# Kernel tuning notes

Hardware: AMD Instinct MI355X
Metric: run time of the kernel (lower is better)

Reference implementation:

```python
import jax, jax.numpy as jnp
import numpy as np

DIM = 784
HEADS = 2
DH = DIM // HEADS  # 392
EPS_LN = 1e-5
EPS_L2 = 1e-12


def layer_norm(x, w, b):
    mu = jnp.mean(x, axis=-1, keepdims=True)
    var = jnp.mean(jnp.square(x - mu), axis=-1, keepdims=True)
    return (x - mu) * jax.lax.rsqrt(var + EPS_LN) * w + b


def hardswish(x):
    return x * jnp.clip(x + 3.0, 0.0, 6.0) / 6.0


def l2norm(x):
    n = jnp.sqrt(jnp.sum(jnp.square(x), axis=-1, keepdims=True))
    return x / jnp.maximum(n, EPS_L2)


def setup_inputs() -> dict:
    key = jax.random.key(0)
    ks = jax.random.split(key, 8)
    B, N = 32, 1024
    x = jax.random.normal(ks[0], (B, N, DIM), dtype=jnp.float32)
    s = 0.02
    qkv_w = jax.random.normal(ks[1], (3 * DIM, DIM), dtype=jnp.float32) * s
    qkv_b = jax.random.normal(ks[2], (3 * DIM,), dtype=jnp.float32) * s
    out_w = jax.random.normal(ks[3], (DIM, DIM), dtype=jnp.float32) * s
    out_b = jax.random.normal(ks[4], (DIM,), dtype=jnp.float32) * s
    ffn_w = jax.random.normal(ks[5], (DIM, DIM), dtype=jnp.float32) * s
    ffn_b = jax.random.normal(ks[6], (DIM,), dtype=jnp.float32) * s
    ln_w = jnp.ones((DIM,), dtype=jnp.float32)
    ln_b = jnp.zeros((DIM,), dtype=jnp.float32)
    scale = jnp.ones((HEADS, 1, 1), dtype=jnp.float32) * 0.01
    return {"x": x, "ln_w": ln_w, "ln_b": ln_b, "qkv_w": qkv_w, "qkv_b": qkv_b,
            "scale": scale, "out_w": out_w, "out_b": out_b, "ffn_w": ffn_w, "ffn_b": ffn_b}


def reference(x, ln_w, ln_b, qkv_w, qkv_b, scale, out_w, out_b, ffn_w, ffn_b):
    B, N, _ = x.shape
    h = HEADS
    xn = layer_norm(x, ln_w, ln_b)
    qkv = xn @ qkv_w.T + qkv_b  # [B, N, 3*DIM]
    q, k, v = jnp.split(qkv, 3, axis=-1)
    # 'b n (h d) -> b h n d'
    def to_heads(t):
        return t.reshape(B, N, h, DH).transpose(0, 2, 1, 3)
    q, k, v = to_heads(q), to_heads(k), to_heads(v)
    q, k = l2norm(q), l2norm(k)
    sim = jnp.einsum('bhnd,bhmd->bhnm', q, k) * jnp.sqrt(scale)  # scale [h,1,1] broadcasts
    attn = jax.nn.softmax(sim, axis=-1)
    out = jnp.einsum('bhnm,bhmd->bhnd', attn, v)
    out = out.transpose(0, 2, 1, 3).reshape(B, N, DIM)  # 'b h n d -> b n (h d)'
    out = layer_norm(out, ln_w, ln_b)  # same LayerNorm params reused
    out = hardswish(out)
    out_ffn = hardswish(out @ ffn_w.T + ffn_b)
    return (out + out_ffn) @ out_w.T + out_b
```

## Files before the change

kernel.cpp:

```cpp
#include <hip/hip_runtime.h>

typedef unsigned short u16;
typedef unsigned int u32;
typedef __attribute__((ext_vector_type(4))) float f32x4;
typedef __attribute__((ext_vector_type(8))) short bf16x8;

#define TOK 32768
#define KP  832
#define DHP 448
#define DHPV 512
#define NQKV 2560

static __device__ __forceinline__ float bf2f(u16 u){ u32 v = ((u32)u)<<16; return __builtin_bit_cast(float, v); }
static __device__ __forceinline__ u16 f2bf(float f){
  u32 x = __builtin_bit_cast(u32, f);
  u32 r = (x + 0x7fffu + ((x>>16)&1u)) >> 16;
  return (u16)r;
}
static __device__ __forceinline__ void gload16(const void* g, void* l){
  __builtin_amdgcn_global_load_lds((const __attribute__((address_space(1))) void*)g,
                                   (__attribute__((address_space(3))) void*)l, 16, 0, 0);
}
static __device__ __forceinline__ float wave_red_sum(float v){
  #pragma unroll
  for (int o = 32; o > 0; o >>= 1) v += __shfl_xor(v, o, 64);
  return v;
}

__global__ __launch_bounds__(256) void wconv_k(const float* __restrict__ src, u16* __restrict__ dst,
                                               int srcR, long long total){
  long long i = (long long)blockIdx.x*256 + threadIdx.x;
  if (i >= total) return;
  int r = (int)(i / KP), c = (int)(i % KP);
  float v = (r < srcR && c < 784) ? src[(long long)r*784 + c] : 0.f;
  dst[i] = f2bf(v);
}

__global__ __launch_bounds__(256) void ln1_k(const float* __restrict__ x, const float* __restrict__ w,
                                             const float* __restrict__ b, u16* __restrict__ out){
  const int tid = threadIdx.x;
  const long long row = blockIdx.x;
  const float* xr = x + row*784;
  float v[4]; float s = 0.f, ss = 0.f;
  #pragma unroll
  for (int i = 0; i < 4; i++){ int c = tid + i*256; float t = (c < 784) ? xr[c] : 0.f; v[i] = t; s += t; ss += t*t; }
  __shared__ float red[8];
  s = wave_red_sum(s); ss = wave_red_sum(ss);
  if ((tid & 63) == 0){ red[tid>>6] = s; red[4 + (tid>>6)] = ss; }
  __syncthreads();
  float S  = red[0]+red[1]+red[2]+red[3];
  float SS = red[4]+red[5]+red[6]+red[7];
  float mean = S * (1.f/784.f);
  float var  = SS * (1.f/784.f) - mean*mean;
  float rstd = rsqrtf(var + 1e-5f);
  u16* orow = out + row*KP;
  #pragma unroll
  for (int i = 0; i < 4; i++){
    int c = tid + i*256;
    if (c < KP){
      u16 o = 0;
      if (c < 784) o = f2bf((v[i]-mean)*rstd*w[c] + b[c]);
      orow[c] = o;
    }
  }
}

__global__ __launch_bounds__(256) void ln2hs_k(const u16* __restrict__ a, const float* __restrict__ w,
                                               const float* __restrict__ b, u16* __restrict__ out){
  const int tid = threadIdx.x;
  const long long row = blockIdx.x;
  const u16* ar = a + row*784;
  float v[4]; float s = 0.f, ss = 0.f;
  #pragma unroll
  for (int i = 0; i < 4; i++){ int c = tid + i*256; float t = (c < 784) ? bf2f(ar[c]) : 0.f; v[i] = t; s += t; ss += t*t; }
  __shared__ float red[8];
  s = wave_red_sum(s); ss = wave_red_sum(ss);
  if ((tid & 63) == 0){ red[tid>>6] = s; red[4 + (tid>>6)] = ss; }
  __syncthreads();
  float S  = red[0]+red[1]+red[2]+red[3];
  float SS = red[4]+red[5]+red[6]+red[7];
  float mean = S * (1.f/784.f);
  float var  = SS * (1.f/784.f) - mean*mean;
  float rstd = rsqrtf(var + 1e-5f);
  u16* orow = out + row*KP;
  #pragma unroll
  for (int i = 0; i < 4; i++){
    int c = tid + i*256;
    if (c < KP){
      u16 o = 0;
      if (c < 784){
        float y = (v[i]-mean)*rstd*w[c] + b[c];
        y = y * fminf(fmaxf(y + 3.f, 0.f), 6.f) * (1.f/6.f);
        o = f2bf(y);
      }
      orow[c] = o;
    }
  }
}

__global__ __launch_bounds__(256) void l2n_k(u16* __restrict__ Q, u16* __restrict__ Kb,
                                             const float* __restrict__ scale){
  const int lane = threadIdx.x & 63, wv = threadIdx.x >> 6;
  const long long rid = (long long)blockIdx.x*4 + wv;
  const bool isK = rid >= 65536;
  const long long idx = isK ? rid - 65536 : rid;
  u16* base = (isK ? Kb : Q) + idx*DHP;
  uint2 t0 = *(const uint2*)(base + lane*4);
  int ch1 = lane + 64;
  uint2 t1 = (ch1 < 112) ? *(const uint2*)(base + ch1*4) : make_uint2(0u,0u);
  float f0[4], f1[4];
  u32 c0[2] = {t0.x, t0.y}, c1[2] = {t1.x, t1.y};
  #pragma unroll
  for (int j = 0; j < 4; j++){
    f0[j] = bf2f((u16)(c0[j>>1] >> ((j&1)*16)));
    f1[j] = bf2f((u16)(c1[j>>1] >> ((j&1)*16)));
  }
  float ssq = 0.f;
  #pragma unroll
  for (int j = 0; j < 4; j++) ssq += f0[j]*f0[j];
  if (ch1 < 98){
    #pragma unroll
    for (int j = 0; j < 4; j++) ssq += f1[j]*f1[j];
  }
  ssq = wave_red_sum(ssq);
  float fac = 1.f / fmaxf(sqrtf(ssq), 1e-12f);
  if (!isK) fac *= sqrtf(scale[(int)((idx >> 10) & 1)]);
  u32 o0[2], o1[2];
  #pragma unroll
  for (int j = 0; j < 2; j++){
    u16 lo = f2bf(f0[2*j]*fac),   hi = f2bf(f0[2*j+1]*fac);
    o0[j] = (u32)lo | ((u32)hi << 16);
    u16 lo1 = (ch1 < 98) ? f2bf(f1[2*j]*fac)   : (u16)0;
    u16 hi1 = (ch1 < 98) ? f2bf(f1[2*j+1]*fac) : (u16)0;
    o1[j] = (u32)lo1 | ((u32)hi1 << 16);
  }
  *(uint2*)(base + lane*4) = make_uint2(o0[0], o0[1]);
  if (ch1 < 112) *(uint2*)(base + ch1*4) = make_uint2(o1[0], o1[1]);
}

__global__ __launch_bounds__(512, 2) void attn_k(const u16* __restrict__ Qb, const u16* __restrict__ Kb,
    const u16* __restrict__ Vtb, u16* __restrict__ att)
{
  __shared__ u16 smem[40960];
  u16* Pbuf = smem + 24576;

  const int tid = threadIdx.x, lane = tid & 63, wid = tid >> 6;
  const int wq  = wid >> 2, kvw = wid & 3;
  const int dw  = wid >> 2, qw  = wid & 3;

  const int lin = (int)blockIdx.x;
  const int bh = (lin & 7)*8 + (lin >> 6);
  const int qt = (lin >> 3) & 7;

  const u16* Qp = Qb  + ((long long)bh*1024 + (long long)qt*128)*DHP;
  const u16* Kp = Kb  + (long long)bh*1024*DHP;
  const u16* Vp = Vtb + (long long)bh*DHPV*1024;

  const int srow = tid >> 2;
  const int scol = (((tid & 3) ^ ((srow >> 1) & 3)) << 3);
  const int s2   = tid + 512;
  const int r2   = s2 >> 2;
  const int c2   = (((s2 & 3) ^ ((r2 >> 1) & 3)) << 3);

  int offq[4], offk[2], offv[7];
  #pragma unroll
  for (int m = 0; m < 4; m++){
    int r = wq*64 + m*16 + (lane & 15);
    offq[m] = r*32 + ((((lane>>4) ^ (r>>1)) & 3) << 3);
  }
  #pragma unroll
  for (int n = 0; n < 2; n++){
    int r = kvw*32 + n*16 + (lane & 15);
    offk[n] = 4096 + r*32 + ((((lane>>4) ^ (r>>1)) & 3) << 3);
  }
  #pragma unroll
  for (int m = 0; m < 7; m++){
    int r = dw*112 + m*16 + (lane & 15);
    offv[m] = r*32 + ((((lane>>4) ^ (r>>1)) & 3) << 3);
  }

  auto stageA = [&](int ck, int t, int buf){
    u16* rb = smem + buf*8192;
    gload16(Qp + (long long)srow*DHP + t*32 + scol,            rb + tid*8);
    gload16(Kp + (long long)(ck*128 + srow)*DHP + t*32 + scol, rb + 4096 + tid*8);
  };
  auto stageV = [&](int ck, int ms, int buf){
    u16* rb = smem + buf*8192;
    const int h = ms >> 2, s = ms & 3;
    const u16* src = Vp + (long long)(h*224)*1024 + ck*128 + s*32;
    gload16(src + (long long)srow*1024 + scol, rb + tid*8);
    gload16(src + (long long)r2*1024  + c2,   rb + s2*8);
  };

  f32x4 oacc[2][7][2];
  #pragma unroll
  for (int h = 0; h < 2; h++)
    #pragma unroll
    for (int m = 0; m < 7; m++)
      #pragma unroll
      for (int n = 0; n < 2; n++) oacc[h][m][n] = f32x4{0.f,0.f,0.f,0.f};
  float rs_r[16];
  #pragma unroll
  for (int i = 0; i < 16; i++) rs_r[i] = 0.f;

  for (int ck = 0; ck < 8; ++ck){
    stageA(ck, 0, 0); stageA(ck, 1, 1);
    asm volatile("s_waitcnt vmcnt(2)" ::: "memory");
    __builtin_amdgcn_s_barrier();
    f32x4 sacc[4][2];
    #pragma unroll
    for (int m = 0; m < 4; m++)
      #pragma unroll
      for (int n = 0; n < 2; n++) sacc[m][n] = f32x4{0.f,0.f,0.f,0.f};

    for (int t = 0; t < 14; ++t){
      if (t + 2 < 14) stageA(ck, t+2, (t+2)%3);
      const u16* ra = smem + (t%3)*8192;
      bf16x8 aq[4], bk[2];
      #pragma unroll
      for (int m = 0; m < 4; m++) aq[m] = *(const bf16x8*)(ra + offq[m]);
      #pragma unroll
      for (int n = 0; n < 2; n++) bk[n] = *(const bf16x8*)(ra + offk[n]);
      __builtin_amdgcn_s_setprio(1);
      #pragma unroll
      for (int m = 0; m < 4; m++)
        #pragma unroll
        for (int n = 0; n < 2; n++)
          sacc[m][n] = __builtin_amdgcn_mfma_f32_16x16x32_bf16(aq[m], bk[n], sacc[m][n], 0, 0, 0);
      __builtin_amdgcn_s_setprio(0);
      if (t + 2 < 14)      asm volatile("s_waitcnt vmcnt(2)" ::: "memory");
      else if (t + 1 < 14) asm volatile("s_waitcnt vmcnt(0)" ::: "memory");
      if (t + 1 < 14) __builtin_amdgcn_s_barrier();
    }
    __builtin_amdgcn_s_barrier();

    stageV(ck, 0, 0); stageV(ck, 1, 1);
    #pragma unroll
    for (int m = 0; m < 4; m++){
      #pragma unroll
      for (int i = 0; i < 4; i++){
        const int q = wq*64 + m*16 + (lane>>4)*4 + i;
        float a = 0.f;
        #pragma unroll
        for (int n = 0; n < 2; n++){
          const int kv = kvw*32 + n*16 + (lane & 15);
          u16 pb = f2bf(__expf(sacc[m][n][i]));
          Pbuf[q*128 + (((kv>>3) ^ (q&15)) << 3) + (kv&7)] = pb;
          a += bf2f(pb);
        }
        rs_r[m*4+i] += a;
      }
    }
    asm volatile("s_waitcnt vmcnt(2) lgkmcnt(0)" ::: "memory");
    __builtin_amdgcn_s_barrier();

    #pragma unroll
    for (int ms = 0; ms < 8; ++ms){
      if (ms + 2 < 8) stageV(ck, ms+2, (ms+2)%3);
      const u16* vb = smem + (ms%3)*8192;
      const int s = ms & 3;
      const int h = ms >> 2;
      bf16x8 av[7], bp[2];
      #pragma unroll
      for (int m = 0; m < 7; m++) av[m] = *(const bf16x8*)(vb + offv[m]);
      #pragma unroll
      for (int n = 0; n < 2; n++){
        const int q = qw*32 + n*16 + (lane & 15);
        const int cc = s*4 + (lane>>4);
        bp[n] = *(const bf16x8*)(Pbuf + q*128 + ((cc ^ (q&15)) << 3));
      }
      __builtin_amdgcn_s_setprio(1);
      #pragma unroll
      for (int m = 0; m < 7; m++)
        #pragma unroll
        for (int n = 0; n < 2; n++)
          oacc[h][m][n] = __builtin_amdgcn_mfma_f32_16x16x32_bf16(av[m], bp[n], oacc[h][m][n], 0, 0, 0);
      __builtin_amdgcn_s_setprio(0);
      if (ms + 2 < 8)      asm volatile("s_waitcnt vmcnt(2)" ::: "memory");
      else if (ms + 1 < 8) asm volatile("s_waitcnt vmcnt(0)" ::: "memory");
      if (ms + 1 < 8) __builtin_amdgcn_s_barrier();
    }
    __builtin_amdgcn_s_barrier();
  }

  float* rsL = (float*)&smem[0];
  float* rsT = rsL + 512;
  #pragma unroll
  for (int m = 0; m < 4; m++){
    #pragma unroll
    for (int i = 0; i < 4; i++){
      float v = rs_r[m*4+i];
      v += __shfl_xor(v, 1, 64); v += __shfl_xor(v, 2, 64);
      v += __shfl_xor(v, 4, 64); v += __shfl_xor(v, 8, 64);
      if ((lane & 15) == 0) rsL[(wq*64 + m*16 + (lane>>4)*4 + i)*4 + kvw] = v;
    }
  }
  __syncthreads();
  if (tid < 128) rsT[tid] = 1.f/(rsL[tid*4]+rsL[tid*4+1]+rsL[tid*4+2]+rsL[tid*4+3]);
  __syncthreads();
  const int b = bh >> 1, hh = bh & 1;
  #pragma unroll
  for (int h = 0; h < 2; h++){
    #pragma unroll
    for (int n = 0; n < 2; n++){
      const int q = qw*32 + n*16 + (lane & 15);
      const float rinv = rsT[q];
      u16* arw = att + ((long long)(b*1024 + qt*128 + q))*784 + hh*392;
      #pragma unroll
      for (int m = 0; m < 7; m++){
        const int d0 = h*224 + dw*112 + m*16 + (lane>>4)*4;
        if (d0 < 392){
          u16 a0 = f2bf(oacc[h][m][n][0]*rinv), a1 = f2bf(oacc[h][m][n][1]*rinv);
          u16 a2 = f2bf(oacc[h][m][n][2]*rinv), a3 = f2bf(oacc[h][m][n][3]*rinv);
          *(u32*)(arw + d0)     = (u32)a0 | ((u32)a1 << 16);
          *(u32*)(arw + d0 + 2) = (u32)a2 | ((u32)a3 << 16);
        }
      }
    }
  }
}

template<int EPI, int ORDER>
__global__ __launch_bounds__(512, 2) void gemm_k(const u16* __restrict__ Ab, const u16* __restrict__ Bb,
    int lda, int ldb, int nkt, long long sA, long long sB,
    const float* __restrict__ fp0, void* __restrict__ vp1, void* __restrict__ vp2, void* __restrict__ vp3)
{
  __shared__ u16 L[4][12288];
  const int tid = threadIdx.x;
  const int lane = tid & 63;
  const int wid = tid >> 6;
  const int wr = wid >> 1, wc = wid & 1;

  const int gx = gridDim.x, gy = gridDim.y;
  const int nwg = gx*gy;
  int lin = (ORDER == 0) ? ((int)blockIdx.x + gx*(int)blockIdx.y)
                         : ((int)blockIdx.y + gy*(int)blockIdx.x);
  const int q8 = nwg >> 3, r8 = nwg & 7;
  const int xcd = lin & 7, base8 = lin >> 3;
  int wg = (xcd < r8 ? xcd*(q8+1) : r8*(q8+1) + (xcd-r8)*q8) + base8;
  int bx, by;
  if (ORDER == 0){ bx = wg % gx; by = wg / gx; }
  else           { by = wg % gy; bx = wg / gy; }

  const u16* A  = Ab + (long long)by*256*lda;
  const u16* Bp = Bb + (long long)bx*128*ldb;

  const int ra0 = tid >> 2;
  const int ka0 = ((((tid) & 3) ^ ((ra0 >> 1) & 3)) << 3);
  const int ra1 = (tid + 512) >> 2;
  const int ka1 = ((((tid + 512) & 3) ^ ((ra1 >> 1) & 3)) << 3);
  const u16* gA0 = A  + (long long)ra0*lda + ka0;
  const u16* gA1 = A  + (long long)ra1*lda + ka1;
  const u16* gB0 = Bp + (long long)ra0*ldb + ka0;

  auto stage = [&](int t, int h){
    const int hb = ((t & 1) << 1) | h;
    u16* dst = &L[hb][0];
    const int k0 = (t << 6) + (h << 5);
    gload16(gA0 + k0, dst + tid*8);
    gload16(gA1 + k0, dst + (tid + 512)*8);
    gload16(gB0 + k0, dst + 8192 + tid*8);
  };

  int offa[4], offb[4];
  #pragma unroll
  for (int m = 0; m < 4; m++){
    int row = wr*64 + m*16 + (lane & 15);
    offa[m] = row*32 + ((((lane >> 4) ^ (row >> 1)) & 3) << 3);
  }
  #pragma unroll
  for (int n = 0; n < 4; n++){
    int row = wc*64 + n*16 + (lane & 15);
    offb[n] = 8192 + row*32 + ((((lane >> 4) ^ (row >> 1)) & 3) << 3);
  }

  f32x4 acc[4][4];
  #pragma unroll
  for (int m = 0; m < 4; m++)
    #pragma unroll
    for (int n = 0; n < 4; n++) acc[m][n] = f32x4{0.f,0.f,0.f,0.f};

  stage(0, 0); stage(0, 1);
  asm volatile("s_waitcnt vmcnt(3)" ::: "memory");
  __builtin_amdgcn_s_barrier();

  for (int t = 0; t < nkt; ++t){
    const bool lastT = (t == nkt - 1);
    #pragma unroll
    for (int h = 0; h < 2; ++h){
      if (!lastT) stage(t + 1, h);
      const int hb = ((t & 1) << 1) | h;
      bf16x8 af[4], bf[4];
      #pragma unroll
      for (int m = 0; m < 4; m++) af[m] = *(const bf16x8*)&L[hb][offa[m]];
      #pragma unroll
      for (int n = 0; n < 4; n++) bf[n] = *(const bf16x8*)&L[hb][offb[n]];
      __builtin_amdgcn_s_setprio(1);
      #pragma unroll
      for (int m = 0; m < 4; m++)
        #pragma unroll
        for (int n = 0; n < 4; n++)
          acc[m][n] = __builtin_amdgcn_mfma_f32_16x16x32_bf16(af[m], bf[n], acc[m][n], 0, 0, 0);
      __builtin_amdgcn_s_setprio(0);
      if (!lastT)          asm volatile("s_waitcnt vmcnt(3)" ::: "memory");
      else if (h == 0)     asm volatile("s_waitcnt vmcnt(0)" ::: "memory");
      if (!(lastT && h == 1)) __builtin_amdgcn_s_barrier();
    }
  }

  const int tm = by*256 + wr*64;
  const int tn = bx*128 + wc*64;

  if constexpr (EPI == 0){
    u16* Qn = (u16*)vp1; u16* Kn = (u16*)vp2; u16* Vt = (u16*)vp3;
    #pragma unroll
    for (int m = 0; m < 4; m++){
      const int row0 = tm + m*16 + (lane>>4)*4;
      if (row0 < 2352){
        const int seg = row0 / 392;
        const int hh = seg & 1;
        const int dd0 = row0 - seg*392;
        const float b0 = fp0[row0], b1 = fp0[row0+1], b2 = fp0[row0+2], b3 = fp0[row0+3];
        #pragma unroll
        for (int n = 0; n < 4; n++){
          const int col = tn + n*16 + (lane&15);
          const int bb = col >> 10, nn = col & 1023;
          if (seg < 4){
            u16* dst = (seg < 2) ? Qn : Kn;
            ushort4 pk;
            pk.x = f2bf(acc[m][n][0] + b0);
            pk.y = f2bf(acc[m][n][1] + b1);
            pk.z = f2bf(acc[m][n][2] + b2);
            pk.w = f2bf(acc[m][n][3] + b3);
            *(ushort4*)(dst + ((long long)((bb*2 + hh)*1024 + nn))*DHP + dd0) = pk;
          } else {
            const long long vb = ((long long)(bb*2 + hh)*DHPV + dd0)*1024 + nn;
            Vt[vb        ] = f2bf(acc[m][n][0] + b0);
            Vt[vb + 1024 ] = f2bf(acc[m][n][1] + b1);
            Vt[vb + 2048 ] = f2bf(acc[m][n][2] + b2);
            Vt[vb + 3072 ] = f2bf(acc[m][n][3] + b3);
          }
        }
      }
    }
  } else {
    #pragma unroll
    for (int m = 0; m < 4; m++){
      #pragma unroll
      for (int n = 0; n < 4; n++){
        #pragma unroll
        for (int i = 0; i < 4; i++){
          const int row = tm + m*16 + (lane>>4)*4 + i;
          const int col = tn + n*16 + (lane&15);
          float v = acc[m][n][i];
          if constexpr (EPI == 4){
            if (col < KP){
              u16 o = 0;
              if (col < 784){
                float f = v + fp0[col];
                f = f * fminf(fmaxf(f + 3.f, 0.f), 6.f) * (1.f/6.f);
                float hv = bf2f(((const u16*)vp1)[(long long)row*KP + col]);
                o = f2bf(hv + f);
              }
              ((u16*)vp2)[(long long)row*KP + col] = o;
            }
          } else {
            if (col < 784){
              ((float*)vp1)[(long long)row*784 + col] = v + fp0[col];
            }
          }
        }
      }
    }
  }
}

extern "C" void kernel_launch(void* const* d_in, const int* in_sizes, int n_in,
                              void* d_out, int out_size, void* d_ws, size_t ws_size,
                              hipStream_t stream)
{
  const float* x     = (const float*)d_in[0];
  const float* ln_w  = (const float*)d_in[1];
  const float* ln_b  = (const float*)d_in[2];
  const float* qkv_w = (const float*)d_in[3];
  const float* qkv_b = (const float*)d_in[4];
  const float* scale = (const float*)d_in[5];
  const float* out_w = (const float*)d_in[6];
  const float* out_b = (const float*)d_in[7];
  const float* ffn_w = (const float*)d_in[8];
  const float* ffn_b = (const float*)d_in[9];

  char* wsp = (char*)d_ws;
  auto alloc = [&](long long bytes)->char*{ char* p = wsp; wsp += (bytes + 255) & ~255LL; return p; };
  u16* XN   = (u16*)alloc((long long)TOK*KP*2);
  u16* WQKV = (u16*)alloc((long long)NQKV*KP*2);
  u16* WFF  = (u16*)alloc(1024LL*KP*2);
  u16* WO   = (u16*)alloc(1024LL*KP*2);
  u16* QN   = (u16*)alloc(64LL*1024*DHP*2);
  u16* KN   = (u16*)alloc(64LL*1024*DHP*2);
  u16* VT   = (u16*)alloc(64LL*DHPV*1024*2);
  u16* ATT = XN;
  u16* H   = QN;
  u16* S   = KN;
  (void)ws_size; (void)in_sizes; (void)n_in; (void)out_size;

  wconv_k<<<dim3(((long long)NQKV*KP + 255)/256), 256, 0, stream>>>(qkv_w, WQKV, 2352, (long long)NQKV*KP);
  wconv_k<<<dim3((1024*KP + 255)/256), 256, 0, stream>>>(ffn_w, WFF, 784, 1024LL*KP);
  wconv_k<<<dim3((1024*KP + 255)/256), 256, 0, stream>>>(out_w, WO,  784, 1024LL*KP);

  ln1_k<<<dim3(TOK), 256, 0, stream>>>(x, ln_w, ln_b, XN);
  gemm_k<0,1><<<dim3(256, 10, 1), 512, 0, stream>>>(WQKV, XN, KP, KP, 13, 0LL, 0LL,
      qkv_b, QN, KN, VT);
  l2n_k<<<dim3(32768), 256, 0, stream>>>(QN, KN, scale);
  attn_k<<<dim3(512), 512, 0, stream>>>(QN, KN, VT, ATT);
  ln2hs_k<<<dim3(TOK), 256, 0, stream>>>(ATT, ln_w, ln_b, H);
  gemm_k<4,0><<<dim3(7, 128, 1), 512, 0, stream>>>(H, WFF, KP, KP, 13, 0LL, 0LL, ffn_b, H, S, nullptr);
  gemm_k<5,0><<<dim3(7, 128, 1), 512, 0, stream>>>(S, WO, KP, KP, 13, 0LL, 0LL, out_b, d_out, nullptr, nullptr);
}
```

Baseline: 719.6 us.

## Deepen GEMM pipeline with register double-buffered LDS fragments and 3-stage prefetch

```diff
diff --git a/kernel.cpp b/kernel.cpp
--- a/kernel.cpp
+++ b/kernel.cpp
@@ -353,10 +353,9 @@
   const u16* gA1 = A  + (long long)ra1*lda + ka1;
   const u16* gB0 = Bp + (long long)ra0*ldb + ka0;
 
-  auto stage = [&](int t, int h){
-    const int hb = ((t & 1) << 1) | h;
-    u16* dst = &L[hb][0];
-    const int k0 = (t << 6) + (h << 5);
+  auto stage = [&](int hp){
+    u16* dst = &L[hp & 3][0];
+    const int k0 = hp << 5;
     gload16(gA0 + k0, dst + tid*8);
     gload16(gA1 + k0, dst + (tid + 512)*8);
     gload16(gB0 + k0, dst + 8192 + tid*8);
@@ -380,32 +379,64 @@
     #pragma unroll
     for (int n = 0; n < 4; n++) acc[m][n] = f32x4{0.f,0.f,0.f,0.f};
 
-  stage(0, 0); stage(0, 1);
+  bf16x8 aX[4], bX[4], aY[4], bY[4];
+
+  auto dsloadX = [&](int hp){
+    const u16* Lb = &L[hp & 3][0];
+    #pragma unroll
+    for (int m = 0; m < 4; m++) aX[m] = *(const bf16x8*)&Lb[offa[m]];
+    #pragma unroll
+    for (int n = 0; n < 4; n++) bX[n] = *(const bf16x8*)&Lb[offb[n]];
+  };
+  auto dsloadY = [&](int hp){
+    const u16* Lb = &L[hp & 3][0];
+    #pragma unroll
+    for (int m = 0; m < 4; m++) aY[m] = *(const bf16x8*)&Lb[offa[m]];
+    #pragma unroll
+    for (int n = 0; n < 4; n++) bY[n] = *(const bf16x8*)&Lb[offb[n]];
+  };
+  auto mfmaX = [&](){
+    __builtin_amdgcn_s_setprio(1);
+    #pragma unroll
+    for (int m = 0; m < 4; m++)
+      #pragma unroll
+      for (int n = 0; n < 4; n++)
+        acc[m][n] = __builtin_amdgcn_mfma_f32_16x16x32_bf16(aX[m], bX[n], acc[m][n], 0, 0, 0);
+    __builtin_amdgcn_s_setprio(0);
+  };
+  auto mfmaY = [&](){
+    __builtin_amdgcn_s_setprio(1);
+    #pragma unroll
+    for (int m = 0; m < 4; m++)
+      #pragma unroll
+      for (int n = 0; n < 4; n++)
+        acc[m][n] = __builtin_amdgcn_mfma_f32_16x16x32_bf16(aY[m], bY[n], acc[m][n], 0, 0, 0);
+    __builtin_amdgcn_s_setprio(0);
+  };
+
+  const int NPH = nkt * 2;
+
+  stage(0); stage(1); stage(2);
   asm volatile("s_waitcnt vmcnt(3)" ::: "memory");
   __builtin_amdgcn_s_barrier();
-
-  for (int t = 0; t < nkt; ++t){
-    const bool lastT = (t == nkt - 1);
-    #pragma unroll
-    for (int h = 0; h < 2; ++h){
-      if (!lastT) stage(t + 1, h);
-      const int hb = ((t & 1) << 1) | h;
-      bf16x8 af[4], bf[4];
-      #pragma unroll
-      for (int m = 0; m < 4; m++) af[m] = *(const bf16x8*)&L[hb][offa[m]];
-      #pragma unroll
-      for (int n = 0; n < 4; n++) bf[n] = *(const bf16x8*)&L[hb][offb[n]];
-      __builtin_amdgcn_s_setprio(1);
-      #pragma unroll
-      for (int m = 0; m < 4; m++)
-        #pragma unroll
-        for (int n = 0; n < 4; n++)
-          acc[m][n] = __builtin_amdgcn_mfma_f32_16x16x32_bf16(af[m], bf[n], acc[m][n], 0, 0, 0);
-      __builtin_amdgcn_s_setprio(0);
-      if (!lastT)          asm volatile("s_waitcnt vmcnt(3)" ::: "memory");
-      else if (h == 0)     asm volatile("s_waitcnt vmcnt(0)" ::: "memory");
-      if (!(lastT && h == 1)) __builtin_amdgcn_s_barrier();
-    }
+  dsloadX(0);
+
+  for (int p = 0; p < NPH; p += 2){
+    if (p + 3 < NPH) stage(p + 3);
+    dsloadY(p + 1);
+    __builtin_amdgcn_sched_barrier(0);
+    mfmaX();
+    if (p + 3 < NPH)      asm volatile("s_waitcnt vmcnt(3)" ::: "memory");
+    else if (p + 2 < NPH) asm volatile("s_waitcnt vmcnt(0)" ::: "memory");
+    __builtin_amdgcn_s_barrier();
+
+    if (p + 4 < NPH) stage(p + 4);
+    if (p + 2 < NPH) dsloadX(p + 2);
+    __builtin_amdgcn_sched_barrier(0);
+    mfmaY();
+    if (p + 4 < NPH)      asm volatile("s_waitcnt vmcnt(3)" ::: "memory");
+    else if (p + 3 < NPH) asm volatile("s_waitcnt vmcnt(0)" ::: "memory");
+    if (p + 2 < NPH) __builtin_amdgcn_s_barrier();
   }
 
   const int tm = by*256 + wr*64;
```

New measurement: 734.5 us. 2.1% more time.

## Enlarge GEMM tile to 256x256 with split A/B staging pipeline

Applied to the files above, without the earlier changes.

```diff
diff --git a/kernel.cpp b/kernel.cpp
--- a/kernel.cpp
+++ b/kernel.cpp
@@ -7,6 +7,7 @@
 
 #define TOK 32768
 #define KP  832
+#define NKT 13
 #define DHP 448
 #define DHPV 512
 #define NQKV 2560
@@ -321,15 +322,15 @@
 }
 
 template<int EPI, int ORDER>
-__global__ __launch_bounds__(512, 2) void gemm_k(const u16* __restrict__ Ab, const u16* __restrict__ Bb,
-    int lda, int ldb, int nkt, long long sA, long long sB,
+__global__ __launch_bounds__(512, 1) void gemm_k(const u16* __restrict__ Ab, const u16* __restrict__ Bb,
+    int lda, int ldb,
     const float* __restrict__ fp0, void* __restrict__ vp1, void* __restrict__ vp2, void* __restrict__ vp3)
 {
-  __shared__ u16 L[4][12288];
+  __shared__ u16 L[8][8192];
   const int tid = threadIdx.x;
   const int lane = tid & 63;
   const int wid = tid >> 6;
-  const int wr = wid >> 1, wc = wid & 1;
+  const int wr = wid >> 2, wc = wid & 3;
 
   const int gx = gridDim.x, gy = gridDim.y;
   const int nwg = gx*gy;
@@ -343,78 +344,136 @@
   else           { by = wg % gy; bx = wg / gy; }
 
   const u16* A  = Ab + (long long)by*256*lda;
-  const u16* Bp = Bb + (long long)bx*128*ldb;
-
-  const int ra0 = tid >> 2;
-  const int ka0 = ((((tid) & 3) ^ ((ra0 >> 1) & 3)) << 3);
-  const int ra1 = (tid + 512) >> 2;
-  const int ka1 = ((((tid + 512) & 3) ^ ((ra1 >> 1) & 3)) << 3);
-  const u16* gA0 = A  + (long long)ra0*lda + ka0;
-  const u16* gA1 = A  + (long long)ra1*lda + ka1;
-  const u16* gB0 = Bp + (long long)ra0*ldb + ka0;
-
-  auto stage = [&](int t, int h){
-    const int hb = ((t & 1) << 1) | h;
-    u16* dst = &L[hb][0];
-    const int k0 = (t << 6) + (h << 5);
-    gload16(gA0 + k0, dst + tid*8);
-    gload16(gA1 + k0, dst + (tid + 512)*8);
-    gload16(gB0 + k0, dst + 8192 + tid*8);
+  const u16* Bp = Bb + (long long)bx*256*ldb;
+
+  const int q1 = tid + 512;
+  const int q0c = (((tid & 3) ^ ((tid >> 3) & 3)) << 3);
+  const int q1c = (((q1  & 3) ^ ((q1  >> 3) & 3)) << 3);
+  const u16* gA0 = A  + (long long)(tid >> 2)*lda + q0c;
+  const u16* gA1 = A  + (long long)(q1  >> 2)*lda + q1c;
+  const u16* gB0 = Bp + (long long)(tid >> 2)*ldb + q0c;
+  const u16* gB1 = Bp + (long long)(q1  >> 2)*ldb + q1c;
+
+  auto stageA = [&](int t, int kh){
+    u16* d = &L[(t & 1)*4 + kh][0];
+    const int k0 = t*64 + kh*32;
+    gload16(gA0 + k0, d + tid*8);
+    gload16(gA1 + k0, d + q1*8);
   };
-
-  int offa[4], offb[4];
-  #pragma unroll
-  for (int m = 0; m < 4; m++){
-    int row = wr*64 + m*16 + (lane & 15);
+  auto stageB = [&](int t, int kh){
+    u16* d = &L[(t & 1)*4 + 2 + kh][0];
+    const int k0 = t*64 + kh*32;
+    gload16(gB0 + k0, d + tid*8);
+    gload16(gB1 + k0, d + q1*8);
+  };
+
+  int offa[8], offb[4];
+  #pragma unroll
+  for (int m = 0; m < 8; m++){
+    int row = wr*128 + m*16 + (lane & 15);
     offa[m] = row*32 + ((((lane >> 4) ^ (row >> 1)) & 3) << 3);
   }
   #pragma unroll
   for (int n = 0; n < 4; n++){
     int row = wc*64 + n*16 + (lane & 15);
-    offb[n] = 8192 + row*32 + ((((lane >> 4) ^ (row >> 1)) & 3) << 3);
-  }
-
-  f32x4 acc[4][4];
-  #pragma unroll
-  for (int m = 0; m < 4; m++)
+    offb[n] = row*32 + ((((lane >> 4) ^ (row >> 1)) & 3) << 3);
+  }
+
+  f32x4 acc[8][4];
+  #pragma unroll
+  for (int m = 0; m < 8; m++)
     #pragma unroll
     for (int n = 0; n < 4; n++) acc[m][n] = f32x4{0.f,0.f,0.f,0.f};
 
-  stage(0, 0); stage(0, 1);
-  asm volatile("s_waitcnt vmcnt(3)" ::: "memory");
+  bf16x8 af[4], bf[4];
+  auto loadA = [&](int t, int kh, int mh){
+    const u16* Lb = &L[(t & 1)*4 + kh][0];
+    af[0] = *(const bf16x8*)&Lb[offa[mh*4 + 0]];
+    af[1] = *(const bf16x8*)&Lb[offa[mh*4 + 1]];
+    af[2] = *(const bf16x8*)&Lb[offa[mh*4 + 2]];
+    af[3] = *(const bf16x8*)&Lb[offa[mh*4 + 3]];
+  };
+  auto loadB = [&](int t, int kh){
+    const u16* Lb = &L[(t & 1)*4 + 2 + kh][0];
+    bf[0] = *(const bf16x8*)&Lb[offb[0]];
+    bf[1] = *(const bf16x8*)&Lb[offb[1]];
+    bf[2] = *(const bf16x8*)&Lb[offb[2]];
+    bf[3] = *(const bf16x8*)&Lb[offb[3]];
+  };
+
+  stageA(0,0); stageB(0,0); stageA(0,1); stageB(0,1); stageA(1,0); stageB(1,0);
+  asm volatile("s_waitcnt vmcnt(8)" ::: "memory");
   __builtin_amdgcn_s_barrier();
 
-  for (int t = 0; t < nkt; ++t){
-    const bool lastT = (t == nkt - 1);
-    #pragma unroll
-    for (int h = 0; h < 2; ++h){
-      if (!lastT) stage(t + 1, h);
-      const int hb = ((t & 1) << 1) | h;
-      bf16x8 af[4], bf[4];
-      #pragma unroll
-      for (int m = 0; m < 4; m++) af[m] = *(const bf16x8*)&L[hb][offa[m]];
-      #pragma unroll
-      for (int n = 0; n < 4; n++) bf[n] = *(const bf16x8*)&L[hb][offb[n]];
-      __builtin_amdgcn_s_setprio(1);
-      #pragma unroll
-      for (int m = 0; m < 4; m++)
-        #pragma unroll
-        for (int n = 0; n < 4; n++)
-          acc[m][n] = __builtin_amdgcn_mfma_f32_16x16x32_bf16(af[m], bf[n], acc[m][n], 0, 0, 0);
-      __builtin_amdgcn_s_setprio(0);
-      if (!lastT)          asm volatile("s_waitcnt vmcnt(3)" ::: "memory");
-      else if (h == 0)     asm volatile("s_waitcnt vmcnt(0)" ::: "memory");
-      if (!(lastT && h == 1)) __builtin_amdgcn_s_barrier();
-    }
-  }
-
-  const int tm = by*256 + wr*64;
-  const int tn = bx*128 + wc*64;
+  for (int t = 0; t < NKT; ++t){
+    loadA(t, 0, 0); loadB(t, 0);
+    if (t + 1 < NKT) stageA(t + 1, 1);
+    __builtin_amdgcn_s_barrier();
+    asm volatile("s_waitcnt lgkmcnt(0)" ::: "memory");
+    __builtin_amdgcn_sched_barrier(0);
+    __builtin_amdgcn_s_setprio(1);
+    #pragma unroll
+    for (int i = 0; i < 4; i++)
+      #pragma unroll
+      for (int n = 0; n < 4; n++)
+        acc[i][n] = __builtin_amdgcn_mfma_f32_16x16x32_bf16(af[i], bf[n], acc[i][n], 0, 0, 0);
+    __builtin_amdgcn_s_setprio(0);
+    __builtin_amdgcn_s_barrier();
+
+    loadA(t, 0, 1);
+    if (t + 1 < NKT) stageB(t + 1, 1);
+    __builtin_amdgcn_s_barrier();
+    asm volatile("s_waitcnt lgkmcnt(0)" ::: "memory");
+    __builtin_amdgcn_sched_barrier(0);
+    __builtin_amdgcn_s_setprio(1);
+    #pragma unroll
+    for (int i = 0; i < 4; i++)
+      #pragma unroll
+      for (int n = 0; n < 4; n++)
+        acc[4+i][n] = __builtin_amdgcn_mfma_f32_16x16x32_bf16(af[i], bf[n], acc[4+i][n], 0, 0, 0);
+    __builtin_amdgcn_s_setprio(0);
+    if (t < NKT-1) asm volatile("s_waitcnt vmcnt(8)" ::: "memory");
+    else           asm volatile("s_waitcnt vmcnt(0)" ::: "memory");
+    __builtin_amdgcn_s_barrier();
+
+    loadA(t, 1, 0); loadB(t, 1);
+    if (t + 2 < NKT) stageA(t + 2, 0);
+    __builtin_amdgcn_s_barrier();
+    asm volatile("s_waitcnt lgkmcnt(0)" ::: "memory");
+    __builtin_amdgcn_sched_barrier(0);
+    __builtin_amdgcn_s_setprio(1);
+    #pragma unroll
+    for (int i = 0; i < 4; i++)
+      #pragma unroll
+      for (int n = 0; n < 4; n++)
+        acc[i][n] = __builtin_amdgcn_mfma_f32_16x16x32_bf16(af[i], bf[n], acc[i][n], 0, 0, 0);
+    __builtin_amdgcn_s_setprio(0);
+    __builtin_amdgcn_s_barrier();
+
+    loadA(t, 1, 1);
+    if (t + 2 < NKT) stageB(t + 2, 0);
+    __builtin_amdgcn_s_barrier();
+    asm volatile("s_waitcnt lgkmcnt(0)" ::: "memory");
+    __builtin_amdgcn_sched_barrier(0);
+    __builtin_amdgcn_s_setprio(1);
+    #pragma unroll
+    for (int i = 0; i < 4; i++)
+      #pragma unroll
+      for (int n = 0; n < 4; n++)
+        acc[4+i][n] = __builtin_amdgcn_mfma_f32_16x16x32_bf16(af[i], bf[n], acc[4+i][n], 0, 0, 0);
+    __builtin_amdgcn_s_setprio(0);
+    if (t < NKT-2)       asm volatile("s_waitcnt vmcnt(8)" ::: "memory");
+    else if (t == NKT-2) asm volatile("s_waitcnt vmcnt(4)" ::: "memory");
+    if (t < NKT-1) __builtin_amdgcn_s_barrier();
+  }
+
+  const int tm = by*256 + wr*128;
+  const int tn = bx*256 + wc*64;
 
   if constexpr (EPI == 0){
     u16* Qn = (u16*)vp1; u16* Kn = (u16*)vp2; u16* Vt = (u16*)vp3;
     #pragma unroll
-    for (int m = 0; m < 4; m++){
+    for (int m = 0; m < 8; m++){
       const int row0 = tm + m*16 + (lane>>4)*4;
       if (row0 < 2352){
         const int seg = row0 / 392;
@@ -445,7 +504,7 @@
     }
   } else {
     #pragma unroll
-    for (int m = 0; m < 4; m++){
+    for (int m = 0; m < 8; m++){
       #pragma unroll
       for (int n = 0; n < 4; n++){
         #pragma unroll
@@ -509,11 +568,10 @@
   wconv_k<<<dim3((1024*KP + 255)/256), 256, 0, stream>>>(out_w, WO,  784, 1024LL*KP);
 
   ln1_k<<<dim3(TOK), 256, 0, stream>>>(x, ln_w, ln_b, XN);
-  gemm_k<0,1><<<dim3(256, 10, 1), 512, 0, stream>>>(WQKV, XN, KP, KP, 13, 0LL, 0LL,
-      qkv_b, QN, KN, VT);
+  gemm_k<0,1><<<dim3(128, 10, 1), 512, 0, stream>>>(WQKV, XN, KP, KP, qkv_b, QN, KN, VT);
   l2n_k<<<dim3(32768), 256, 0, stream>>>(QN, KN, scale);
   attn_k<<<dim3(512), 512, 0, stream>>>(QN, KN, VT, ATT);
   ln2hs_k<<<dim3(TOK), 256, 0, stream>>>(ATT, ln_w, ln_b, H);
-  gemm_k<4,0><<<dim3(7, 128, 1), 512, 0, stream>>>(H, WFF, KP, KP, 13, 0LL, 0LL, ffn_b, H, S, nullptr);
-  gemm_k<5,0><<<dim3(7, 128, 1), 512, 0, stream>>>(S, WO, KP, KP, 13, 0LL, 0LL, out_b, d_out, nullptr, nullptr);
-}
+  gemm_k<4,0><<<dim3(4, 128, 1), 512, 0, stream>>>(H, WFF, KP, KP, ffn_b, H, S, nullptr);
+  gemm_k<5,0><<<dim3(4, 128, 1), 512, 0, stream>>>(S, WO, KP, KP, out_b, d_out, nullptr, nullptr);
+}
```

Measured after the change: 714.4 us. No clear change (-0.7%).
